# Optimization experiments

Measured on AMD Instinct MI355X. Metric: run time of the kernel, lower is better.

The kernel has to match this reference:

```python
import jax, jax.numpy as jnp
import numpy as np

B, S, D = 2, 2048, 2048
H, KV, HD = 16, 8, 128
EPS = 1e-6
NEG = -1e9


def rms_norm(x, w, eps=EPS):
    # per-head RMSNorm over last dim, computed in fp32 like the torch module
    xf = x.astype(jnp.float32)
    var = jnp.mean(xf * xf, axis=-1, keepdims=True)
    return (w * (xf * jax.lax.rsqrt(var + eps)).astype(x.dtype))


def rotate_half(x):
    x1, x2 = jnp.split(x, 2, axis=-1)
    return jnp.concatenate((-x2, x1), axis=-1)


def setup_inputs() -> dict:
    key = jax.random.key(0)
    ks = jax.random.split(key, 8)
    hidden_states = jax.random.normal(ks[0], (B, S, D), dtype=jnp.float32)
    # RoPE tables (rope_theta=10000), shape [B, S, HD]
    inv_freq = 1.0 / (10000.0 ** (np.arange(0, HD, 2, dtype=np.float32) / HD))
    t = np.arange(S, dtype=np.float32)
    freqs = np.outer(t, inv_freq)                      # [S, HD/2]
    emb = np.concatenate([freqs, freqs], axis=-1)      # [S, HD]
    cos = jnp.broadcast_to(jnp.cos(emb)[None], (B, S, HD)).astype(jnp.float32)
    sin = jnp.broadcast_to(jnp.sin(emb)[None], (B, S, HD)).astype(jnp.float32)
    # additive causal mask [B, 1, S, S]
    causal = jnp.triu(jnp.full((S, S), NEG, dtype=jnp.float32), k=1)
    attention_mask = jnp.broadcast_to(causal[None, None], (B, 1, S, S))
    scale = 0.02
    Wq = jax.random.normal(ks[1], (D, H * HD), dtype=jnp.float32) * scale
    Wk = jax.random.normal(ks[2], (D, KV * HD), dtype=jnp.float32) * scale
    Wv = jax.random.normal(ks[3], (D, KV * HD), dtype=jnp.float32) * scale
    Wo = jax.random.normal(ks[4], (H * HD, D), dtype=jnp.float32) * scale
    q_norm_w = jnp.ones((HD,), dtype=jnp.float32)
    k_norm_w = jnp.ones((HD,), dtype=jnp.float32)
    return {"hidden_states": hidden_states, "cos": cos, "sin": sin,
            "attention_mask": attention_mask, "Wq": Wq, "Wk": Wk, "Wv": Wv,
            "Wo": Wo, "q_norm_w": q_norm_w, "k_norm_w": k_norm_w}


def reference(hidden_states, cos, sin, attention_mask, Wq, Wk, Wv, Wo, q_norm_w, k_norm_w):
    b, s, _ = hidden_states.shape
    scaling = HD ** -0.5
    n_rep = H // KV
    q = (hidden_states @ Wq).reshape(b, s, H, HD)
    k = (hidden_states @ Wk).reshape(b, s, KV, HD)
    v = (hidden_states @ Wv).reshape(b, s, KV, HD)
    # per-head RMSNorm then [B, heads, S, HD]
    q = rms_norm(q, q_norm_w).transpose(0, 2, 1, 3)
    k = rms_norm(k, k_norm_w).transpose(0, 2, 1, 3)
    v = v.transpose(0, 2, 1, 3)
    # RoPE (cos/sin unsqueezed on head axis)
    c = cos[:, None, :, :]
    sn = sin[:, None, :, :]
    q = q * c + rotate_half(q) * sn
    k = k * c + rotate_half(k) * sn
    # GQA: repeat kv heads
    k = jnp.repeat(k, n_rep, axis=1)
    v = jnp.repeat(v, n_rep, axis=1)
    scores = jnp.einsum('bhqd,bhkd->bhqk', q, k) * scaling + attention_mask
    probs = jax.nn.softmax(scores.astype(jnp.float32), axis=-1).astype(q.dtype)
    out = jnp.einsum('bhqk,bhkd->bhqd', probs, v)
    out = out.transpose(0, 2, 1, 3).reshape(b, s, H * HD)
    return out @ Wo
```

## Files before the change

### kernel.cpp

```cpp
#include <hip/hip_runtime.h>

typedef unsigned short u16;
typedef unsigned short u16x8 __attribute__((ext_vector_type(8)));
typedef unsigned short u16x4 __attribute__((ext_vector_type(4)));
typedef short s16x8 __attribute__((ext_vector_type(8)));
typedef float f32x4 __attribute__((ext_vector_type(4)));
typedef float f32x16 __attribute__((ext_vector_type(16)));
typedef unsigned u32x4 __attribute__((ext_vector_type(4)));

__device__ __forceinline__ u16 f2b(float f){
  unsigned u = __builtin_bit_cast(unsigned, f);
  u += 0x7fffu + ((u >> 16) & 1u);
  return (u16)(u >> 16);
}
__device__ __forceinline__ float b2f(u16 v){
  unsigned u = ((unsigned)v) << 16;
  return __builtin_bit_cast(float, u);
}

#define MFMA16(c, a, b) (c) = __builtin_amdgcn_mfma_f32_16x16x32_bf16((a), (b), (c), 0, 0, 0)
#define MFMA32(c, a, b) (c) = __builtin_amdgcn_mfma_f32_32x32x16_bf16((a), (b), (c), 0, 0, 0)

__device__ __forceinline__ void gl16(const u16* g, char* l){
  __builtin_amdgcn_global_load_lds((const __attribute__((address_space(1))) void*)g,
                                   (__attribute__((address_space(3))) void*)l, 16, 0, 0);
}

__global__ void k_cast(const float* __restrict__ src, u16* __restrict__ dst, int n8){
  int i = blockIdx.x * blockDim.x + threadIdx.x;
  if (i >= n8) return;
  const float4* s = (const float4*)(src + (size_t)i * 8);
  float4 a = s[0], b = s[1];
  u16x8 o;
  o[0]=f2b(a.x); o[1]=f2b(a.y); o[2]=f2b(a.z); o[3]=f2b(a.w);
  o[4]=f2b(b.x); o[5]=f2b(b.y); o[6]=f2b(b.z); o[7]=f2b(b.w);
  *(u16x8*)(dst + (size_t)i * 8) = o;
}

__global__ void k_transall(const float* __restrict__ Wq, const float* __restrict__ Wk,
                           const float* __restrict__ Wv, const float* __restrict__ Wo,
                           u16* __restrict__ wqkvT, u16* __restrict__ woT){
  __shared__ float t[32][33];
  int by = blockIdx.y;
  const float* src; u16* dst; int N;
  if (by < 64)       { src = Wq; dst = wqkvT;                        N = 2048; }
  else if (by < 128) { src = Wk; dst = wqkvT + (size_t)2048 * 2048;  N = 1024; by -= 64; }
  else if (by < 192) { src = Wv; dst = wqkvT + (size_t)3072 * 2048;  N = 1024; by -= 128; }
  else               { src = Wo; dst = woT;                          N = 2048; by -= 192; }
  int n0 = blockIdx.x * 32, k0 = by * 32;
  if (n0 >= N) return;
  int c = threadIdx.x & 31, r4 = threadIdx.x >> 5;
  #pragma unroll
  for (int p = 0; p < 4; ++p){
    int r = r4 + p * 8;
    t[r][c] = src[(size_t)(k0 + r) * N + n0 + c];
  }
  __syncthreads();
  #pragma unroll
  for (int p = 0; p < 4; ++p){
    int r = r4 + p * 8;
    dst[(size_t)(n0 + r) * 2048 + k0 + c] = f2b(t[c][r]);
  }
}

template<int NREP, int MODE>
__global__ __launch_bounds__(512, 1) void k_gemm8(const u16* __restrict__ A, const u16* __restrict__ BT,
                                                  float* __restrict__ Cv, int M, int N, int K,
                                                  u16* __restrict__ qout, u16* __restrict__ kout,
                                                  u16* __restrict__ vout,
                                                  const float* __restrict__ cosT, const float* __restrict__ sinT,
                                                  const float* __restrict__ qw, const float* __restrict__ kw){
  constexpr int NH = NREP / 2;
  constexpr int BROWS = NREP * 32;
  constexpr int BLOADS = NREP / 2;
  constexpr int TOT = 4 + 2 * BLOADS;
  constexpr int SMEM = 65536 + 2 * 2 * BROWS * 64 * 2;
  __shared__ __align__(128) char smem[SMEM];
  u16* sAp = (u16*)smem;
  u16* sBp = (u16*)(smem + 65536);
  const int tid = threadIdx.x;
  const int lane = tid & 63, w = tid >> 6;
  const int l15 = lane & 15, l4 = lane >> 4;
  const int sx = l15 & 7;
  const int wr = w >> 2, wc = w & 3;
  const int m0 = blockIdx.y * 256, n0 = blockIdx.x * (NREP * 64);
  const int nk = K >> 6;

  f32x4 acc[8][NREP];
  #pragma unroll
  for (int mi = 0; mi < 8; ++mi)
    #pragma unroll
    for (int ni = 0; ni < NREP; ++ni) acc[mi][ni] = (f32x4){0.f, 0.f, 0.f, 0.f};

  auto stageA = [&](int d, int half, int k0){
    #pragma unroll
    for (int j = 0; j < 2; ++j){
      const int q = j * 512 + tid;
      const int r = q >> 3, cc = q & 7;
      gl16(A + (size_t)(m0 + half * 128 + r) * K + k0 + ((cc ^ (r & 7)) << 3),
           (char*)(sAp + (d * 2 + half) * 8192) + j * 8192 + (tid >> 6) * 1024);
    }
  };
  auto stageB = [&](int d, int half, int k0){
    #pragma unroll
    for (int j = 0; j < BLOADS; ++j){
      const int q = j * 512 + tid;
      const int r = q >> 3, cc = q & 7;
      gl16(BT + (size_t)(n0 + half * BROWS + r) * K + k0 + ((cc ^ (r & 7)) << 3),
           (char*)(sBp + (d * 2 + half) * (BROWS * 64)) + j * 8192 + (tid >> 6) * 1024);
    }
  };

  stageA(0, 0, 0); stageA(0, 1, 0); stageB(0, 0, 0); stageB(0, 1, 0);
  stageA(1, 0, 64); stageA(1, 1, 64); stageB(1, 0, 64); stageB(1, 1, 64);
  if constexpr (TOT == 8) asm volatile("s_waitcnt vmcnt(8)" ::: "memory");
  else                    asm volatile("s_waitcnt vmcnt(6)" ::: "memory");
  __builtin_amdgcn_s_barrier();

  const int halfB = wc >> 1;
  const int rb0 = (wc & 1) * (NREP * 16);

  for (int kt = 0; kt < nk; ++kt){
    const int d = kt & 1;
    const bool pre = (kt + 2) < nk;
    const int k0n = (kt + 2) << 6;
    const char* hA = (const char*)(sAp + (d * 2 + wr) * 8192);
    const char* hB = (const char*)(sBp + (d * 2 + halfB) * (BROWS * 64));
    s16x8 aa[4][2], bb0[NH][2], bb1[NH][2];

    #pragma unroll
    for (int mi = 0; mi < 4; ++mi)
      #pragma unroll
      for (int kk = 0; kk < 2; ++kk)
        aa[mi][kk] = *(const s16x8*)(hA + (mi * 16 + l15) * 128 + (((kk * 4 + l4) ^ sx) << 4));
    #pragma unroll
    for (int ni = 0; ni < NH; ++ni)
      #pragma unroll
      for (int kk = 0; kk < 2; ++kk)
        bb0[ni][kk] = *(const s16x8*)(hB + (rb0 + ni * 16 + l15) * 128 + (((kk * 4 + l4) ^ sx) << 4));
    __builtin_amdgcn_s_setprio(1);
    #pragma unroll
    for (int mi = 0; mi < 4; ++mi)
      #pragma unroll
      for (int ni = 0; ni < NH; ++ni)
        #pragma unroll
        for (int kk = 0; kk < 2; ++kk)
          MFMA16(acc[mi][ni], aa[mi][kk], bb0[ni][kk]);
    __builtin_amdgcn_s_setprio(0);

    #pragma unroll
    for (int ni = 0; ni < NH; ++ni)
      #pragma unroll
      for (int kk = 0; kk < 2; ++kk)
        bb1[ni][kk] = *(const s16x8*)(hB + (rb0 + (NH + ni) * 16 + l15) * 128 + (((kk * 4 + l4) ^ sx) << 4));
    __builtin_amdgcn_s_setprio(1);
    #pragma unroll
    for (int mi = 0; mi < 4; ++mi)
      #pragma unroll
      for (int ni = 0; ni < NH; ++ni)
        #pragma unroll
        for (int kk = 0; kk < 2; ++kk)
          MFMA16(acc[mi][NH + ni], aa[mi][kk], bb1[ni][kk]);
    __builtin_amdgcn_s_setprio(0);
    __builtin_amdgcn_s_barrier();

    #pragma unroll
    for (int mi = 0; mi < 4; ++mi)
      #pragma unroll
      for (int kk = 0; kk < 2; ++kk)
        aa[mi][kk] = *(const s16x8*)(hA + ((mi + 4) * 16 + l15) * 128 + (((kk * 4 + l4) ^ sx) << 4));
    if (pre){ stageB(d, 0, k0n); stageB(d, 1, k0n); }
    __builtin_amdgcn_s_setprio(1);
    #pragma unroll
    for (int mi = 0; mi < 4; ++mi)
      #pragma unroll
      for (int ni = 0; ni < NH; ++ni)
        #pragma unroll
        for (int kk = 0; kk < 2; ++kk)
          MFMA16(acc[mi + 4][ni], aa[mi][kk], bb0[ni][kk]);
    __builtin_amdgcn_s_setprio(0);
    __builtin_amdgcn_s_barrier();

    if (pre){ stageA(d, 0, k0n); stageA(d, 1, k0n); }
    __builtin_amdgcn_s_setprio(1);
    #pragma unroll
    for (int mi = 0; mi < 4; ++mi)
      #pragma unroll
      for (int ni = 0; ni < NH; ++ni)
        #pragma unroll
        for (int kk = 0; kk < 2; ++kk)
          MFMA16(acc[mi + 4][NH + ni], aa[mi][kk], bb1[ni][kk]);
    __builtin_amdgcn_s_setprio(0);
    if (kt + 1 < nk){
      if (pre){
        if constexpr (TOT == 8) asm volatile("s_waitcnt vmcnt(8)" ::: "memory");
        else                    asm volatile("s_waitcnt vmcnt(6)" ::: "memory");
      } else {
        asm volatile("s_waitcnt vmcnt(0)" ::: "memory");
      }
      __builtin_amdgcn_s_barrier();
    }
  }

  if constexpr (MODE == 0){
    #pragma unroll
    for (int mi = 0; mi < 8; ++mi)
      #pragma unroll
      for (int ni = 0; ni < NREP; ++ni)
        #pragma unroll
        for (int i = 0; i < 4; ++i){
          const int row = m0 + wr * 128 + mi * 16 + l4 * 4 + i;
          const int col = n0 + wc * (NREP * 16) + ni * 16 + l15;
          Cv[(size_t)row * N + col] = acc[mi][ni][i];
        }
  } else {
    const int u    = (n0 >> 7) + (wc >> 1);
    const int half = wc & 1;
    __syncthreads();
    float ss[32];
    if (u < 24){
      #pragma unroll
      for (int mi = 0; mi < 8; ++mi)
        #pragma unroll
        for (int i = 0; i < 4; ++i){
          float s2 = 0.f;
          #pragma unroll
          for (int ni = 0; ni < 4; ++ni){ float x = acc[mi][ni][i]; s2 += x * x; }
          ss[mi * 4 + i] = s2;
        }
      #pragma unroll
      for (int off = 1; off < 16; off <<= 1)
        #pragma unroll
        for (int r = 0; r < 32; ++r) ss[r] += __shfl_xor(ss[r], off);
      float* sums = (float*)smem;
      if (l15 == 0){
        #pragma unroll
        for (int mi = 0; mi < 8; ++mi)
          #pragma unroll
          for (int i = 0; i < 4; ++i)
            sums[(wr * 4 + wc) * 128 + mi * 16 + l4 * 4 + i] = ss[mi * 4 + i];
      }
    } else {
      #pragma unroll
      for (int mi = 0; mi < 8; ++mi)
        #pragma unroll
        for (int ni = 0; ni < 4; ++ni)
          #pragma unroll
          for (int i = 0; i < 4; ++i){
            const int rowi = m0 + wr * 128 + mi * 16 + l4 * 4 + i;
            const int b_ = rowi >> 11, s_ = rowi & 2047;
            const int d = half * 64 + ni * 16 + l15;
            vout[((size_t)(b_ * 8 + (u - 24)) * 2048 + s_) * 128 + d] = f2b(acc[mi][ni][i]);
          }
    }
    __syncthreads();
    if (u < 24){
      const float* sums = (const float*)smem;
      #pragma unroll
      for (int mi = 0; mi < 8; ++mi)
        #pragma unroll
        for (int i = 0; i < 4; ++i){
          float tot = ss[mi * 4 + i] + sums[(wr * 4 + (wc ^ 1)) * 128 + mi * 16 + l4 * 4 + i];
          ss[mi * 4 + i] = rsqrtf(tot * (1.0f / 128.0f) + 1e-6f);
        }
      const float* wvp = (u < 16) ? qw : kw;
      float wn[4];
      #pragma unroll
      for (int ni = 0; ni < 4; ++ni) wn[ni] = wvp[half * 64 + ni * 16 + l15];
      #pragma unroll
      for (int mi = 0; mi < 8; ++mi)
        #pragma unroll
        for (int ni = 0; ni < 4; ++ni)
          #pragma unroll
          for (int i = 0; i < 4; ++i)
            acc[mi][ni][i] *= ss[mi * 4 + i] * wn[ni];
    }
    __syncthreads();
    u16* scr = (u16*)smem;
    if (u < 24){
      #pragma unroll
      for (int mi = 0; mi < 8; ++mi)
        #pragma unroll
        for (int ni = 0; ni < 4; ++ni){
          u16x4 pk;
          #pragma unroll
          for (int i = 0; i < 4; ++i) pk[i] = f2b(acc[mi][ni][i]);
          *(u16x4*)(scr + ((((wr * 4 + wc) * 8 + mi) * 4 + ni) * 256) + (l4 * 16 + l15) * 4) = pk;
        }
    }
    __syncthreads();
    if (u < 24){
      #pragma unroll
      for (int mi = 0; mi < 8; ++mi){
        #pragma unroll
        for (int ni = 0; ni < 4; ++ni){
          u16x4 pk = *(const u16x4*)(scr + ((((wr * 4 + (wc ^ 1)) * 8 + mi) * 4 + ni) * 256) + (l4 * 16 + l15) * 4);
          const int d = half * 64 + ni * 16 + l15;
          #pragma unroll
          for (int i = 0; i < 4; ++i){
            const int rowi = m0 + wr * 128 + mi * 16 + l4 * 4 + i;
            const int b_ = rowi >> 11, s_ = rowi & 2047;
            const float cs = cosT[(size_t)rowi * 128 + d];
            const float sn = sinT[(size_t)rowi * 128 + d];
            const float self = acc[mi][ni][i];
            const float part = b2f(pk[i]);
            const float o = half ? (self * cs + part * sn) : (self * cs - part * sn);
            if (u < 16) qout[((size_t)(b_ * 16 + u) * 2048 + s_) * 128 + d] = f2b(o);
            else        kout[((size_t)(b_ * 8 + (u - 16)) * 2048 + s_) * 128 + d] = f2b(o);
          }
        }
      }
    }
  }
}

__global__ __launch_bounds__(256, 8) void k_vtrans(const u16* __restrict__ v, u16* __restrict__ vt){
  __shared__ u16 t[64][130];
  const int bid = blockIdx.x;
  const int hd = bid >> 5, sb = bid & 31;
  const u16* src = v + (size_t)hd * 262144 + (size_t)sb * 64 * 128;
  u16* dst = vt + (size_t)hd * 262144 + sb * 64;
  const int tid = threadIdx.x;
  const int r = tid >> 2, c0 = (tid & 3) * 32;
  #pragma unroll
  for (int j = 0; j < 4; ++j)
    *(u16x8*)&t[r][c0 + j * 8] = *(const u16x8*)(src + r * 128 + c0 + j * 8);
  __syncthreads();
  const int d = tid >> 1, s0 = (tid & 1) * 32;
  #pragma unroll
  for (int j = 0; j < 4; ++j){
    u16x8 ov;
    #pragma unroll
    for (int e = 0; e < 8; ++e) ov[e] = t[s0 + j * 8 + e][d];
    *(u16x8*)(dst + (size_t)d * 2048 + s0 + j * 8) = ov;
  }
}

__device__ __forceinline__ void stage_kv(const u16* __restrict__ Kg, const u16* __restrict__ Vt,
                                         int kt, u16* sKb, u16* sVb, int tid){
  #pragma unroll
  for (int i = 0; i < 4; ++i){
    const int off = i * 4096 + tid * 16;
    const unsigned wub = (unsigned)(i * 4096 + (tid >> 6) * 1024);
    const int key = off >> 8, ks = (off >> 4) & 15;
    __builtin_amdgcn_global_load_lds(
        (const __attribute__((address_space(1))) void*)(Kg + (size_t)(kt * 64 + key) * 128 + ((ks ^ (key & 15)) << 3)),
        (__attribute__((address_space(3))) void*)((char*)sKb + wub), 16, 0, 0);
    const int d = off >> 7, vs = (off >> 4) & 7;
    __builtin_amdgcn_global_load_lds(
        (const __attribute__((address_space(1))) void*)(Vt + (size_t)d * 2048 + kt * 64 + ((vs ^ (d & 7)) << 3)),
        (__attribute__((address_space(3))) void*)((char*)sVb + wub), 16, 0, 0);
  }
}

__global__ __launch_bounds__(256, 2) void k_attn(const u16* __restrict__ qb, const u16* __restrict__ kb,
                                                 const u16* __restrict__ vtb, u16* __restrict__ ob){
  __shared__ __align__(128) u16 sK[2][64 * 128];
  __shared__ __align__(128) u16 sV[2][128 * 64];
  const int tid = threadIdx.x, lane = tid & 63, w = tid >> 6;
  const int hi = lane >> 5, l31 = lane & 31;
  const int bid = blockIdx.x;
  const int bh = bid & 31;
  const int kvh = bh & 7, r2 = bh >> 3;
  const int b = r2 >> 1, h = kvh * 2 + (r2 & 1);
  const int slot = bid >> 5;
  const int qt = (slot < 8) ? (15 - 2 * slot) : (2 * slot - 16);
  const u16* Q  = qb  + ((size_t)(b * 16 + h)  * 2048) * 128;
  const u16* Kg = kb  + ((size_t)(b * 8 + kvh) * 2048) * 128;
  const u16* Vt = vtb + ((size_t)(b * 8 + kvh) * 128) * 2048;
  const int qrow0 = qt * 128 + w * 32;

  s16x8 qf[8];
  #pragma unroll
  for (int ds = 0; ds < 8; ++ds)
    qf[ds] = *(const s16x8*)(Q + (size_t)(qrow0 + l31) * 128 + ds * 16 + hi * 8);

  f32x16 acc[4] = {};
  float mx = -1e30f, lsum = 0.f;
  const int nkt = qt * 2 + 2;

  stage_kv(Kg, Vt, 0, sK[0], sV[0], tid);
  for (int kt = 0; kt < nkt; ++kt){
    const int cur = kt & 1;
    if (kt + 1 < nkt){
      stage_kv(Kg, Vt, kt + 1, sK[cur ^ 1], sV[cur ^ 1], tid);
      asm volatile("s_waitcnt vmcnt(8)");
    } else {
      asm volatile("s_waitcnt vmcnt(0)");
    }
    __builtin_amdgcn_s_barrier();

    if (kt * 64 <= qrow0 + 31){
      const char* sKc = (const char*)sK[cur];
      const char* sVc = (const char*)sV[cur];
      f32x16 s0 = {}, s1 = {};
      #pragma unroll
      for (int ds = 0; ds < 8; ++ds){
        const int sl = ((ds * 2 + hi) ^ (l31 & 15)) << 4;
        s16x8 k0 = *(const s16x8*)(sKc + l31 * 256 + sl);
        s16x8 k1 = *(const s16x8*)(sKc + 8192 + l31 * 256 + sl);
        MFMA32(s0, k0, qf[ds]);
        MFMA32(s1, k1, qf[ds]);
      }
      const int qg = qrow0 + l31;
      const bool domask = (kt * 64 + 63) > qrow0;
      float pv0[16], pv1[16];
      float pmax = -1e30f;
      #pragma unroll
      for (int r = 0; r < 16; ++r){
        const int krow = (r & 3) + 8 * (r >> 2) + 4 * hi;
        float v0 = s0[r] * 0.08838834764831845f;
        float v1 = s1[r] * 0.08838834764831845f;
        if (domask){
          if (kt * 64 + krow > qg)      v0 = -1e30f;
          if (kt * 64 + 32 + krow > qg) v1 = -1e30f;
        }
        pv0[r] = v0; pv1[r] = v1;
        pmax = fmaxf(pmax, fmaxf(v0, v1));
      }
      pmax = fmaxf(pmax, __shfl_xor(pmax, 32));
      if (!__all(pmax - mx <= 8.f)){
        const float mn = fmaxf(mx, pmax);
        const float al = __expf(mx - mn);
        mx = mn; lsum *= al;
        #pragma unroll
        for (int r = 0; r < 16; ++r){
          const float ar = __shfl(al, (r & 3) + 8 * (r >> 2) + 4 * hi);
          acc[0][r] *= ar; acc[1][r] *= ar; acc[2][r] *= ar; acc[3][r] *= ar;
        }
      }
      float rs = 0.f;
      #pragma unroll
      for (int r = 0; r < 16; ++r){
        const float e0 = __expf(pv0[r] - mx);
        const float e1 = __expf(pv1[r] - mx);
        pv0[r] = e0; pv1[r] = e1;
        rs += e0 + e1;
      }
      rs += __shfl_xor(rs, 32);
      lsum += rs;
      #pragma unroll
      for (int s = 0; s < 4; ++s){
        const int t8 = (s & 1) * 8;
        unsigned w0, w1, w2, w3;
        if (s < 2){
          asm("v_cvt_pk_bf16_f32 %0, %1, %2" : "=v"(w0) : "v"(pv0[t8+0]), "v"(pv0[t8+1]));
          asm("v_cvt_pk_bf16_f32 %0, %1, %2" : "=v"(w1) : "v"(pv0[t8+2]), "v"(pv0[t8+3]));
          asm("v_cvt_pk_bf16_f32 %0, %1, %2" : "=v"(w2) : "v"(pv0[t8+4]), "v"(pv0[t8+5]));
          asm("v_cvt_pk_bf16_f32 %0, %1, %2" : "=v"(w3) : "v"(pv0[t8+6]), "v"(pv0[t8+7]));
        } else {
          asm("v_cvt_pk_bf16_f32 %0, %1, %2" : "=v"(w0) : "v"(pv1[t8+0]), "v"(pv1[t8+1]));
          asm("v_cvt_pk_bf16_f32 %0, %1, %2" : "=v"(w1) : "v"(pv1[t8+2]), "v"(pv1[t8+3]));
          asm("v_cvt_pk_bf16_f32 %0, %1, %2" : "=v"(w2) : "v"(pv1[t8+4]), "v"(pv1[t8+5]));
          asm("v_cvt_pk_bf16_f32 %0, %1, %2" : "=v"(w3) : "v"(pv1[t8+6]), "v"(pv1[t8+7]));
        }
        asm("v_permlane32_swap_b32 %0, %1" : "+v"(w0), "+v"(w2));
        asm("v_permlane32_swap_b32 %0, %1" : "+v"(w1), "+v"(w3));
        u32x4 pw = {w0, w1, w2, w3};
        s16x8 pa = __builtin_bit_cast(s16x8, pw);
        #pragma unroll
        for (int db = 0; db < 4; ++db){
          const int d = db * 32 + l31;
          s16x8 vf = *(const s16x8*)(sVc + d * 128 + (((s * 2 + hi) ^ (d & 7)) << 4));
          MFMA32(acc[db], pa, vf);
        }
      }
    }
    asm volatile("s_waitcnt lgkmcnt(0)");
    __builtin_amdgcn_s_barrier();
  }
  float li[16];
  #pragma unroll
  for (int r = 0; r < 16; ++r)
    li[r] = __shfl(lsum, (r & 3) + 8 * (r >> 2) + 4 * hi);
  #pragma unroll
  for (int db = 0; db < 4; ++db)
    #pragma unroll
    for (int r = 0; r < 16; ++r){
      const int row = qrow0 + (r & 3) + 8 * (r >> 2) + 4 * hi;
      const int col = h * 128 + db * 32 + l31;
      ob[((size_t)(b * 2048) + row) * 2048 + col] = f2b(acc[db][r] / li[r]);
    }
}

extern "C" void kernel_launch(void* const* d_in, const int* in_sizes, int n_in,
                              void* d_out, int out_size, void* d_ws, size_t ws_size,
                              hipStream_t stream){
  const float* hs   = (const float*)d_in[0];
  const float* cosT = (const float*)d_in[1];
  const float* sinT = (const float*)d_in[2];
  const float* Wq = (const float*)d_in[4];
  const float* Wk = (const float*)d_in[5];
  const float* Wv = (const float*)d_in[6];
  const float* Wo = (const float*)d_in[7];
  const float* qw = (const float*)d_in[8];
  const float* kw = (const float*)d_in[9];
  float* out = (float*)d_out;
  char* ws = (char*)d_ws;

  u16* hsb   = (u16*)(ws);
  u16* wqkvT = (u16*)(ws + ((size_t)16 << 20));
  u16* woT   = (u16*)(ws + ((size_t)32 << 20));
  u16* qb    = (u16*)(ws + ((size_t)40 << 20));
  u16* kb2   = (u16*)(ws + ((size_t)56 << 20));
  u16* vb2   = (u16*)(ws + ((size_t)64 << 20));
  u16* vtb   = (u16*)(ws + ((size_t)72 << 20));
  u16* attnb = (u16*)(ws + ((size_t)80 << 20));

  k_cast<<<4096, 256, 0, stream>>>(hs, hsb, 1048576);
  k_transall<<<dim3(64, 256), 256, 0, stream>>>(Wq, Wk, Wv, Wo, wqkvT, woT);
  k_gemm8<4, 1><<<dim3(16, 16), 512, 0, stream>>>(hsb, wqkvT, nullptr, 4096, 4096, 2048,
                                                  qb, kb2, vb2, cosT, sinT, qw, kw);
  k_vtrans<<<512, 256, 0, stream>>>(vb2, vtb);
  k_attn<<<512, 256, 0, stream>>>(qb, kb2, vtb, attnb);
  k_gemm8<2, 0><<<dim3(16, 16), 512, 0, stream>>>(attnb, woT, (float*)out, 4096, 2048, 2048,
                                                  nullptr, nullptr, nullptr, nullptr, nullptr, nullptr, nullptr);
}
```

Baseline: 209.6 us.

## Stage GEMM epilogues through LDS and fuse V transpose into QKV GEMM

The QKV GEMM epilogue now writes normalized Q/K tiles into swizzled shared memory and reads them back as full rows, so RoPE is applied with vectorized 16-byte loads and stores instead of scattered scalar writes. V tiles are stored transposed in LDS and written straight to the transposed V layout, which removes the separate k_vtrans kernel and its extra round trip through global memory. The output GEMM epilogue also stages fp32 results through LDS to produce coalesced float4 stores. Shared memory grows to at least 128 KB per block, which may limit occupancy, although launch bounds already force one block per CU.

```diff
diff --git a/kernel.cpp b/kernel.cpp
--- a/kernel.cpp
+++ b/kernel.cpp
@@ -74,7 +74,8 @@
   constexpr int BROWS = NREP * 32;
   constexpr int BLOADS = NREP / 2;
   constexpr int TOT = 4 + 2 * BLOADS;
-  constexpr int SMEM = 65536 + 2 * 2 * BROWS * 64 * 2;
+  constexpr int SMEM0 = 65536 + 2 * 2 * BROWS * 64 * 2;
+  constexpr int SMEM = (SMEM0 > 131072) ? SMEM0 : 131072;
   __shared__ __align__(128) char smem[SMEM];
   u16* sAp = (u16*)smem;
   u16* sBp = (u16*)(smem + 65536);
@@ -203,22 +204,36 @@
   }
 
   if constexpr (MODE == 0){
+    float* fOut = (float*)smem;
+    __syncthreads();
     #pragma unroll
     for (int mi = 0; mi < 8; ++mi)
       #pragma unroll
       for (int ni = 0; ni < NREP; ++ni)
         #pragma unroll
         for (int i = 0; i < 4; ++i){
-          const int row = m0 + wr * 128 + mi * 16 + l4 * 4 + i;
-          const int col = n0 + wc * (NREP * 16) + ni * 16 + l15;
-          Cv[(size_t)row * N + col] = acc[mi][ni][i];
-        }
+          const int rl = wr * 128 + mi * 16 + l4 * 4 + i;
+          const int cl = wc * (NREP * 16) + ni * 16 + l15;
+          fOut[rl * 128 + (cl ^ ((rl & 7) << 2))] = acc[mi][ni][i];
+        }
+    __syncthreads();
+    const int c0 = (tid & 31) * 4;
+    const int rb = (tid >> 5) & 15;
+    #pragma unroll
+    for (int j = 0; j < 16; ++j){
+      const int rl = rb + j * 16;
+      f32x4 vv = *(const f32x4*)(fOut + rl * 128 + (c0 ^ ((rl & 7) << 2)));
+      *(f32x4*)(Cv + (size_t)(m0 + rl) * N + n0 + c0) = vv;
+    }
   } else {
-    const int u    = (n0 >> 7) + (wc >> 1);
+    const int u0 = n0 >> 7;
+    const int type = (u0 >= 24) ? 2 : ((u0 >= 16) ? 1 : 0);
+    const int uiw = wc >> 1;
     const int half = wc & 1;
+    u16* sOut = (u16*)smem;
     __syncthreads();
     float ss[32];
-    if (u < 24){
+    if (type < 2){
       #pragma unroll
       for (int mi = 0; mi < 8; ++mi)
         #pragma unroll
@@ -240,21 +255,9 @@
           for (int i = 0; i < 4; ++i)
             sums[(wr * 4 + wc) * 128 + mi * 16 + l4 * 4 + i] = ss[mi * 4 + i];
       }
-    } else {
-      #pragma unroll
-      for (int mi = 0; mi < 8; ++mi)
-        #pragma unroll
-        for (int ni = 0; ni < 4; ++ni)
-          #pragma unroll
-          for (int i = 0; i < 4; ++i){
-            const int rowi = m0 + wr * 128 + mi * 16 + l4 * 4 + i;
-            const int b_ = rowi >> 11, s_ = rowi & 2047;
-            const int d = half * 64 + ni * 16 + l15;
-            vout[((size_t)(b_ * 8 + (u - 24)) * 2048 + s_) * 128 + d] = f2b(acc[mi][ni][i]);
-          }
     }
     __syncthreads();
-    if (u < 24){
+    if (type < 2){
       const float* sums = (const float*)smem;
       #pragma unroll
       for (int mi = 0; mi < 8; ++mi)
@@ -263,7 +266,7 @@
           float tot = ss[mi * 4 + i] + sums[(wr * 4 + (wc ^ 1)) * 128 + mi * 16 + l4 * 4 + i];
           ss[mi * 4 + i] = rsqrtf(tot * (1.0f / 128.0f) + 1e-6f);
         }
-      const float* wvp = (u < 16) ? qw : kw;
+      const float* wvp = (type == 0) ? qw : kw;
       float wn[4];
       #pragma unroll
       for (int ni = 0; ni < 4; ++ni) wn[ni] = wvp[half * 64 + ni * 16 + l15];
@@ -276,63 +279,78 @@
             acc[mi][ni][i] *= ss[mi * 4 + i] * wn[ni];
     }
     __syncthreads();
-    u16* scr = (u16*)smem;
-    if (u < 24){
+    if (type < 2){
       #pragma unroll
       for (int mi = 0; mi < 8; ++mi)
         #pragma unroll
+        for (int ni = 0; ni < 4; ++ni)
+          #pragma unroll
+          for (int i = 0; i < 4; ++i){
+            const int rl = wr * 128 + mi * 16 + l4 * 4 + i;
+            const int d  = half * 64 + ni * 16 + l15;
+            sOut[(uiw * 256 + rl) * 128 + (d ^ ((rl & 7) << 3))] = f2b(acc[mi][ni][i]);
+          }
+    } else {
+      #pragma unroll
+      for (int mi = 0; mi < 8; ++mi)
+        #pragma unroll
         for (int ni = 0; ni < 4; ++ni){
+          const int r0 = wr * 128 + mi * 16 + l4 * 4;
+          const int d  = half * 64 + ni * 16 + l15;
           u16x4 pk;
           #pragma unroll
           for (int i = 0; i < 4; ++i) pk[i] = f2b(acc[mi][ni][i]);
-          *(u16x4*)(scr + ((((wr * 4 + wc) * 8 + mi) * 4 + ni) * 256) + (l4 * 16 + l15) * 4) = pk;
+          *(u16x4*)(sOut + (uiw * 128 + d) * 256 + (r0 ^ ((d & 15) << 4))) = pk;
         }
     }
     __syncthreads();
-    if (u < 24){
-      #pragma unroll
-      for (int mi = 0; mi < 8; ++mi){
-        #pragma unroll
-        for (int ni = 0; ni < 4; ++ni){
-          u16x4 pk = *(const u16x4*)(scr + ((((wr * 4 + (wc ^ 1)) * 8 + mi) * 4 + ni) * 256) + (l4 * 16 + l15) * 4);
-          const int d = half * 64 + ni * 16 + l15;
-          #pragma unroll
-          for (int i = 0; i < 4; ++i){
-            const int rowi = m0 + wr * 128 + mi * 16 + l4 * 4 + i;
-            const int b_ = rowi >> 11, s_ = rowi & 2047;
-            const float cs = cosT[(size_t)rowi * 128 + d];
-            const float sn = sinT[(size_t)rowi * 128 + d];
-            const float self = acc[mi][ni][i];
-            const float part = b2f(pk[i]);
-            const float o = half ? (self * cs + part * sn) : (self * cs - part * sn);
-            if (u < 16) qout[((size_t)(b_ * 16 + u) * 2048 + s_) * 128 + d] = f2b(o);
-            else        kout[((size_t)(b_ * 8 + (u - 16)) * 2048 + s_) * 128 + d] = f2b(o);
-          }
-        }
-      }
-    }
-  }
-}
-
-__global__ __launch_bounds__(256, 8) void k_vtrans(const u16* __restrict__ v, u16* __restrict__ vt){
-  __shared__ u16 t[64][130];
-  const int bid = blockIdx.x;
-  const int hd = bid >> 5, sb = bid & 31;
-  const u16* src = v + (size_t)hd * 262144 + (size_t)sb * 64 * 128;
-  u16* dst = vt + (size_t)hd * 262144 + sb * 64;
-  const int tid = threadIdx.x;
-  const int r = tid >> 2, c0 = (tid & 3) * 32;
-  #pragma unroll
-  for (int j = 0; j < 4; ++j)
-    *(u16x8*)&t[r][c0 + j * 8] = *(const u16x8*)(src + r * 128 + c0 + j * 8);
-  __syncthreads();
-  const int d = tid >> 1, s0 = (tid & 1) * 32;
-  #pragma unroll
-  for (int j = 0; j < 4; ++j){
-    u16x8 ov;
-    #pragma unroll
-    for (int e = 0; e < 8; ++e) ov[e] = t[s0 + j * 8 + e][d];
-    *(u16x8*)(dst + (size_t)d * 2048 + s0 + j * 8) = ov;
+    const int b_  = m0 >> 11;
+    const int s0_ = m0 & 2047;
+    if (type < 2){
+      const int uix = tid >> 8;
+      const int d0  = (tid & 15) * 8;
+      const int rb  = (tid >> 4) & 15;
+      const int u_  = u0 + uix;
+      const float sg = (d0 < 64) ? -1.f : 1.f;
+      u16* outp = (type == 0)
+        ? qout + ((size_t)(b_ * 16 + u_) * 2048 + s0_) * 128
+        : kout + ((size_t)(b_ * 8 + (u_ - 16)) * 2048 + s0_) * 128;
+      #pragma unroll
+      for (int j = 0; j < 16; ++j){
+        const int rl = rb + j * 16;
+        const int rowi = m0 + rl;
+        const int sw = (rl & 7) << 3;
+        u16x8 xs = *(const u16x8*)(sOut + (uix * 256 + rl) * 128 + (d0 ^ sw));
+        u16x8 xp = *(const u16x8*)(sOut + (uix * 256 + rl) * 128 + ((d0 ^ 64) ^ sw));
+        const float* cp = cosT + (size_t)rowi * 128 + d0;
+        const float* sp = sinT + (size_t)rowi * 128 + d0;
+        float4 ca = *(const float4*)cp,  cb = *(const float4*)(cp + 4);
+        float4 sa = *(const float4*)sp,  sb = *(const float4*)(sp + 4);
+        float cv[8] = {ca.x, ca.y, ca.z, ca.w, cb.x, cb.y, cb.z, cb.w};
+        float sv[8] = {sa.x, sa.y, sa.z, sa.w, sb.x, sb.y, sb.z, sb.w};
+        u16x8 o;
+        #pragma unroll
+        for (int e = 0; e < 8; ++e)
+          o[e] = f2b(b2f(xs[e]) * cv[e] + sg * b2f(xp[e]) * sv[e]);
+        *(u16x8*)(outp + (size_t)rl * 128 + d0) = o;
+      }
+    } else {
+      const int rc = tid & 31;
+      const int dq = (tid >> 5) & 15;
+      const int r0g = rc * 8;
+      #pragma unroll
+      for (int ui2 = 0; ui2 < 2; ++ui2){
+        const int vh = u0 + ui2 - 24;
+        u16* dv = vout + ((size_t)(b_ * 8 + vh) * 128) * 2048 + s0_;
+        #pragma unroll
+        for (int dl = 0; dl < 8; ++dl){
+          const int d = dq * 8 + dl;
+          const int r0s = r0g ^ ((d & 15) << 4);
+          u16x8 vv = *(const u16x8*)(sOut + (ui2 * 128 + d) * 256 + r0s);
+          *(u16x8*)(dv + (size_t)d * 2048 + r0g) = vv;
+        }
+      }
+    }
   }
 }
 
@@ -503,15 +521,13 @@
   u16* woT   = (u16*)(ws + ((size_t)32 << 20));
   u16* qb    = (u16*)(ws + ((size_t)40 << 20));
   u16* kb2   = (u16*)(ws + ((size_t)56 << 20));
-  u16* vb2   = (u16*)(ws + ((size_t)64 << 20));
-  u16* vtb   = (u16*)(ws + ((size_t)72 << 20));
-  u16* attnb = (u16*)(ws + ((size_t)80 << 20));
+  u16* vtb   = (u16*)(ws + ((size_t)64 << 20));
+  u16* attnb = (u16*)(ws + ((size_t)72 << 20));
 
   k_cast<<<4096, 256, 0, stream>>>(hs, hsb, 1048576);
   k_transall<<<dim3(64, 256), 256, 0, stream>>>(Wq, Wk, Wv, Wo, wqkvT, woT);
   k_gemm8<4, 1><<<dim3(16, 16), 512, 0, stream>>>(hsb, wqkvT, nullptr, 4096, 4096, 2048,
-                                                  qb, kb2, vb2, cosT, sinT, qw, kw);
-  k_vtrans<<<512, 256, 0, stream>>>(vb2, vtb);
+                                                  qb, kb2, vtb, cosT, sinT, qw, kw);
   k_attn<<<512, 256, 0, stream>>>(qb, kb2, vtb, attnb);
   k_gemm8<2, 0><<<dim3(16, 16), 512, 0, stream>>>(attnb, woT, (float*)out, 4096, 2048, 2048,
                                                   nullptr, nullptr, nullptr, nullptr, nullptr, nullptr, nullptr);
```

Result: faster. 204.9 us (median of 2 runs) (-2.2%).
